# Optimization experiments

Hardware: AMD Instinct MI355X
Metric: run time of the kernel (lower is better)

The kernel has to match this reference:

```python
import jax, jax.numpy as jnp
import numpy as np

IN_FEATURES = 1024
ACT_BITS = 4


def _hadamard(size: int) -> np.ndarray:
    # Sylvester construction, normalized: H(n) = Sylvester(n) / sqrt(n)
    h = np.array([[1.0]], dtype=np.float64)
    while h.shape[0] < size:
        h = np.block([[h, h], [h, -h]])
    return (h / np.sqrt(size)).astype(np.float32)


def _quantize_activations(x, bits=ACT_BITS):
    pos = 2 ** (bits - 1) - 1  # 7
    neg = 2 ** (bits - 1)      # 8
    scale = jnp.clip(jnp.max(jnp.abs(jax.lax.stop_gradient(x)), axis=-1, keepdims=True), 1e-5) / pos
    q = jnp.clip(jnp.round(x / scale), -neg, pos) * scale
    return x + jax.lax.stop_gradient(q - x)  # STE


def _ternary_quantize_ste(w):
    scale = jnp.clip(jnp.mean(jnp.abs(jax.lax.stop_gradient(w)), axis=1, keepdims=True), 1e-5)
    n = w / scale
    tern = jnp.where(n > 0.5, 1.0, jnp.where(n < -0.5, -1.0, 0.0))
    q = tern * scale
    return w + jax.lax.stop_gradient(q - w)  # STE


def setup_inputs() -> dict:
    key = jax.random.key(0)
    k1, k2 = jax.random.split(key)
    x = jax.random.normal(k1, (8, 8192, IN_FEATURES), dtype=jnp.float32)
    # master weight ~ kaiming-uniform-ish scale
    bound = 1.0 / np.sqrt(IN_FEATURES)
    weight = jax.random.uniform(k2, (1024, IN_FEATURES), dtype=jnp.float32, minval=-bound, maxval=bound)
    return {"x": x, "weight": weight}


def reference(x, weight):
    H = jnp.asarray(_hadamard(IN_FEATURES))  # [in, in]
    xh = x @ H                                # Hadamard precondition on input
    xq = _quantize_activations(xh)            # per-token 4-bit symmetric quant (STE)
    wq = _ternary_quantize_ste(weight)        # per-row ternary quant (STE)
    return jnp.einsum('bsi,oi->bso', xq, wq)  # F.linear, no bias
```

## Files before the change

### kernel.cpp

```cpp
#include <hip/hip_runtime.h>
#include <stdint.h>

typedef int v4i __attribute__((ext_vector_type(4)));
typedef float float4_t __attribute__((ext_vector_type(4)));

#define K_DIM 1024
#define N_DIM 1024
#define BM 128
#define BN 128

__device__ __forceinline__ void gload16(const void* g, void* l) {
  __builtin_amdgcn_global_load_lds(
      (const __attribute__((address_space(1))) unsigned int*)g,
      (__attribute__((address_space(3))) unsigned int*)l, 16, 0, 0);
}

#define MFMA_I8 __builtin_amdgcn_mfma_i32_16x16x64_i8

__global__ __launch_bounds__(256) void fwht_quant_kernel(
    const float* __restrict__ x, int8_t* __restrict__ qx,
    float* __restrict__ ascale, int M) {
  const int lane = threadIdx.x & 63;
  const int wid = threadIdx.x >> 6;
  const long token = (long)blockIdx.x * 4 + wid;
  if (token >= M) return;
  const float4_t* xr4 = (const float4_t*)(x + token * K_DIM);

  float v[16];
#pragma unroll
  for (int i = 0; i < 4; ++i) {
    float4_t f = xr4[lane * 4 + i];
#pragma unroll
    for (int c = 0; c < 4; ++c) v[i * 4 + c] = f[c];
  }
#pragma unroll
  for (int s = 1; s <= 8; s <<= 1) {
#pragma unroll
    for (int r = 0; r < 16; ++r)
      if ((r & s) == 0) {
        float a0 = v[r], b0 = v[r | s];
        v[r] = a0 + b0;
        v[r | s] = a0 - b0;
      }
  }
#pragma unroll
  for (int m = 1; m <= 32; m <<= 1) {
    const float sg = (lane & m) ? -1.0f : 1.0f;
#pragma unroll
    for (int r = 0; r < 16; ++r) {
      float p = __shfl_xor(v[r], m, 64);
      v[r] = fmaf(sg, v[r], p);
    }
  }
  float mx = 0.f;
#pragma unroll
  for (int r = 0; r < 16; ++r) mx = fmaxf(mx, fabsf(v[r]));
#pragma unroll
  for (int m = 32; m >= 1; m >>= 1) mx = fmaxf(mx, __shfl_xor(mx, m, 64));
  const float scale = fmaxf(mx * 0.03125f, 1e-5f) * (1.0f / 7.0f);
  if (lane == 0) ascale[token] = scale;
  const float inv = 0.03125f / scale;

  v4i pk;
#pragma unroll
  for (int i = 0; i < 4; ++i) {
    int packed = 0;
#pragma unroll
    for (int c = 0; c < 4; ++c) {
      float q = rintf(v[i * 4 + c] * inv);
      q = fminf(7.f, fmaxf(-8.f, q));
      packed |= ((int)q & 0xff) << (8 * c);
    }
    pk[i] = packed;
  }
  *(v4i*)(qx + token * K_DIM + lane * 16) = pk;
}

__global__ __launch_bounds__(256) void wquant_kernel(
    const float* __restrict__ w, int8_t* __restrict__ qw,
    float* __restrict__ wscale) {
  const int lane = threadIdx.x & 63;
  const int wid = threadIdx.x >> 6;
  const int row = blockIdx.x * 4 + wid;
  const float* wr = w + (long)row * K_DIM;

  float v[16];
  float s = 0.f;
  const float4_t* wr4 = (const float4_t*)wr;
#pragma unroll
  for (int rr = 0; rr < 4; ++rr) {
    float4_t f = wr4[rr * 64 + lane];
#pragma unroll
    for (int c = 0; c < 4; ++c) {
      v[rr * 4 + c] = f[c];
      s += fabsf(f[c]);
    }
  }
#pragma unroll
  for (int m = 32; m >= 1; m >>= 1) s += __shfl_xor(s, m, 64);
  const float scale = fmaxf(s * (1.0f / 1024.0f), 1e-5f);
  if (lane == 0) wscale[row] = scale;

  int8_t* qr = qw + (long)row * K_DIM;
#pragma unroll
  for (int rr = 0; rr < 4; ++rr) {
    int packed = 0;
#pragma unroll
    for (int c = 0; c < 4; ++c) {
      float n = v[rr * 4 + c] / scale;
      int t = (n > 0.5f) ? 1 : ((n < -0.5f) ? -1 : 0);
      packed |= (t & 0xff) << (8 * c);
    }
    *(int*)(qr + rr * 256 + lane * 4) = packed;
  }
}

__global__ __launch_bounds__(256) void gemm_i8_kernel(
    const int8_t* __restrict__ A, const int8_t* __restrict__ B,
    const float* __restrict__ asc, const float* __restrict__ wsc,
    float* __restrict__ C, int M) {
  __shared__ __align__(16) int8_t smem[34816];
  int8_t* Al = smem;
  int8_t* Bl = smem + 16384;
  float* tr = (float*)smem;

  const int t = threadIdx.x;
  const int lane = t & 63;
  const int wm = (t >> 6) >> 1;
  const int wn = (t >> 6) & 1;
  const int rl = lane & 15;
  const int kb = lane >> 4;

  const int swz = ((int)blockIdx.x & 7) * 512 + ((int)blockIdx.x >> 3);
  const long bm = swz >> 3;
  const int bn = swz & 7;

  const int chunkoff = (((t & 7) ^ ((t >> 3) & 7)) << 4);
  const int8_t* gA = A + (bm * BM + (t >> 3)) * (long)K_DIM + chunkoff;
  const int8_t* gB = B + ((long)bn * BN + (t >> 3)) * K_DIM + chunkoff;

  const int sw0 = ((kb ^ (rl & 7)) << 4);
  const int sw1 = (((4 + kb) ^ (rl & 7)) << 4);
  const int arow = (wm * 64 + rl) * 128;
  const int brow = (wn * 64 + rl) * 128;

  v4i acc[4][4] = {};

  for (int ks = 0; ks < K_DIM; ks += 128) {
    gload16(gA + ks, Al + t * 16);
    gload16(gA + ks + 32 * K_DIM, Al + 4096 + t * 16);
    gload16(gA + ks + 64 * K_DIM, Al + 8192 + t * 16);
    gload16(gA + ks + 96 * K_DIM, Al + 12288 + t * 16);
    gload16(gB + ks, Bl + t * 16);
    gload16(gB + ks + 32 * K_DIM, Bl + 4096 + t * 16);
    gload16(gB + ks + 64 * K_DIM, Bl + 8192 + t * 16);
    gload16(gB + ks + 96 * K_DIM, Bl + 12288 + t * 16);
    __syncthreads();

#pragma unroll
    for (int ks2 = 0; ks2 < 2; ++ks2) {
      const int sw = ks2 ? sw1 : sw0;
      v4i a[4], b[4];
#pragma unroll
      for (int i = 0; i < 4; ++i)
        a[i] = *(const v4i*)(Al + arow + i * 2048 + sw);
#pragma unroll
      for (int j = 0; j < 4; ++j)
        b[j] = *(const v4i*)(Bl + brow + j * 2048 + sw);
#pragma unroll
      for (int i = 0; i < 4; ++i)
#pragma unroll
        for (int j = 0; j < 4; ++j)
          acc[i][j] = MFMA_I8(a[i], b[j], acc[i][j], 0, 0, 0);
    }
    __syncthreads();
  }

  const long rowg0 = bm * BM + wm * 64;
  const int colg0 = bn * BN + wn * 64;
#pragma unroll
  for (int c = 0; c < 2; ++c) {
    if (wm == c) {
#pragma unroll
      for (int i = 0; i < 4; ++i) {
        float as[4];
#pragma unroll
        for (int r = 0; r < 4; ++r) as[r] = asc[rowg0 + i * 16 + kb * 4 + r];
#pragma unroll
        for (int j = 0; j < 4; ++j) {
          const float ws = wsc[colg0 + j * 16 + rl];
#pragma unroll
          for (int r = 0; r < 4; ++r)
            tr[(i * 16 + kb * 4 + r) * 132 + wn * 64 + j * 16 + rl] =
                (float)acc[i][j][r] * as[r] * ws;
        }
      }
    }
    __syncthreads();
#pragma unroll
    for (int it = 0; it < 8; ++it) {
      const int idx = t + it * 256;
      const int rl2 = idx >> 5;
      const int c4 = (idx & 31) * 4;
      const float4_t val = *(const float4_t*)(tr + rl2 * 132 + c4);
      __builtin_nontemporal_store(
          val, (float4_t*)(C + (bm * BM + c * 64 + rl2) * (long)N_DIM + bn * BN + c4));
    }
    __syncthreads();
  }
}

extern "C" void kernel_launch(void* const* d_in, const int* in_sizes, int n_in,
                              void* d_out, int out_size, void* d_ws, size_t ws_size,
                              hipStream_t stream) {
  const float* x = (const float*)d_in[0];
  const float* w = (const float*)d_in[1];
  float* out = (float*)d_out;
  const int M = in_sizes[0] / K_DIM;

  int8_t* qx = (int8_t*)d_ws;
  int8_t* qw = qx + (size_t)M * K_DIM;
  float* ascale = (float*)(qw + (size_t)N_DIM * K_DIM);
  float* wscale = ascale + M;

  fwht_quant_kernel<<<(M + 3) / 4, 256, 0, stream>>>(x, qx, ascale, M);
  wquant_kernel<<<N_DIM / 4, 256, 0, stream>>>(w, qw, wscale);
  gemm_i8_kernel<<<(M / BM) * (N_DIM / BN), 256, 0, stream>>>(qx, qw, ascale, wscale, out, M);
}
```

Before: 172.8 us.

## Fuse Hadamard transform and activation quantization into the int8 GEMM kernel

Removes the standalone FWHT+quantize kernel and the int8 activation round trip through global memory. Each 512-thread block now transforms and quantizes a 64-token slab straight into LDS, keeping the whole K dimension resident. It then streams all 1024 weight columns through double-buffered LDS tiles, writing 64x128 output tiles as it goes. This cuts global traffic and one launch, but the smaller M tile means less MFMA reuse per B load, and each block reads all of B. The large LDS footprint limits occupancy to one block per CU.

```diff
diff --git a/kernel.cpp b/kernel.cpp
--- a/kernel.cpp
+++ b/kernel.cpp
@@ -6,8 +6,7 @@
 
 #define K_DIM 1024
 #define N_DIM 1024
-#define BM 128
-#define BN 128
+#define TOK 64
 
 __device__ __forceinline__ void gload16(const void* g, void* l) {
   __builtin_amdgcn_global_load_lds(
@@ -16,65 +15,6 @@
 }
 
 #define MFMA_I8 __builtin_amdgcn_mfma_i32_16x16x64_i8
-
-__global__ __launch_bounds__(256) void fwht_quant_kernel(
-    const float* __restrict__ x, int8_t* __restrict__ qx,
-    float* __restrict__ ascale, int M) {
-  const int lane = threadIdx.x & 63;
-  const int wid = threadIdx.x >> 6;
-  const long token = (long)blockIdx.x * 4 + wid;
-  if (token >= M) return;
-  const float4_t* xr4 = (const float4_t*)(x + token * K_DIM);
-
-  float v[16];
-#pragma unroll
-  for (int i = 0; i < 4; ++i) {
-    float4_t f = xr4[lane * 4 + i];
-#pragma unroll
-    for (int c = 0; c < 4; ++c) v[i * 4 + c] = f[c];
-  }
-#pragma unroll
-  for (int s = 1; s <= 8; s <<= 1) {
-#pragma unroll
-    for (int r = 0; r < 16; ++r)
-      if ((r & s) == 0) {
-        float a0 = v[r], b0 = v[r | s];
-        v[r] = a0 + b0;
-        v[r | s] = a0 - b0;
-      }
-  }
-#pragma unroll
-  for (int m = 1; m <= 32; m <<= 1) {
-    const float sg = (lane & m) ? -1.0f : 1.0f;
-#pragma unroll
-    for (int r = 0; r < 16; ++r) {
-      float p = __shfl_xor(v[r], m, 64);
-      v[r] = fmaf(sg, v[r], p);
-    }
-  }
-  float mx = 0.f;
-#pragma unroll
-  for (int r = 0; r < 16; ++r) mx = fmaxf(mx, fabsf(v[r]));
-#pragma unroll
-  for (int m = 32; m >= 1; m >>= 1) mx = fmaxf(mx, __shfl_xor(mx, m, 64));
-  const float scale = fmaxf(mx * 0.03125f, 1e-5f) * (1.0f / 7.0f);
-  if (lane == 0) ascale[token] = scale;
-  const float inv = 0.03125f / scale;
-
-  v4i pk;
-#pragma unroll
-  for (int i = 0; i < 4; ++i) {
-    int packed = 0;
-#pragma unroll
-    for (int c = 0; c < 4; ++c) {
-      float q = rintf(v[i * 4 + c] * inv);
-      q = fminf(7.f, fmaxf(-8.f, q));
-      packed |= ((int)q & 0xff) << (8 * c);
-    }
-    pk[i] = packed;
-  }
-  *(v4i*)(qx + token * K_DIM + lane * 16) = pk;
-}
 
 __global__ __launch_bounds__(256) void wquant_kernel(
     const float* __restrict__ w, int8_t* __restrict__ qw,
@@ -108,106 +48,177 @@
 #pragma unroll
     for (int c = 0; c < 4; ++c) {
       float n = v[rr * 4 + c] / scale;
-      int t = (n > 0.5f) ? 1 : ((n < -0.5f) ? -1 : 0);
-      packed |= (t & 0xff) << (8 * c);
+      int tv = (n > 0.5f) ? 1 : ((n < -0.5f) ? -1 : 0);
+      packed |= (tv & 0xff) << (8 * c);
     }
     *(int*)(qr + rr * 256 + lane * 4) = packed;
   }
 }
 
-__global__ __launch_bounds__(256) void gemm_i8_kernel(
-    const int8_t* __restrict__ A, const int8_t* __restrict__ B,
-    const float* __restrict__ asc, const float* __restrict__ wsc,
-    float* __restrict__ C, int M) {
-  __shared__ __align__(16) int8_t smem[34816];
-  int8_t* Al = smem;
-  int8_t* Bl = smem + 16384;
-  float* tr = (float*)smem;
+__global__ __launch_bounds__(512) void fused_fwht_gemm_kernel(
+    const float* __restrict__ x, const int8_t* __restrict__ Bq,
+    const float* __restrict__ wsc, float* __restrict__ C) {
+  __shared__ __align__(16) int8_t smem[132352];
+  int8_t* At = smem;
+  int8_t* Bb0 = smem + 65536;
+  int8_t* Bb1 = smem + 81920;
+  float* tr = (float*)(smem + 98304);
+  float* ascl = (float*)(smem + 132096);
 
   const int t = threadIdx.x;
   const int lane = t & 63;
-  const int wm = (t >> 6) >> 1;
-  const int wn = (t >> 6) & 1;
+  const int wid = t >> 6;
+  const int wm = wid >> 2;
+  const int wn = wid & 3;
   const int rl = lane & 15;
   const int kb = lane >> 4;
-
-  const int swz = ((int)blockIdx.x & 7) * 512 + ((int)blockIdx.x >> 3);
-  const long bm = swz >> 3;
-  const int bn = swz & 7;
+  const long bm = blockIdx.x;
+
+  {
+    const float4_t* xb = (const float4_t*)(x + bm * TOK * (long)K_DIM);
+    int token = wid * 8;
+    float4_t f0 = xb[(long)token * 256 + lane * 4 + 0];
+    float4_t f1 = xb[(long)token * 256 + lane * 4 + 1];
+    float4_t f2 = xb[(long)token * 256 + lane * 4 + 2];
+    float4_t f3 = xb[(long)token * 256 + lane * 4 + 3];
+    for (int tk = 0; tk < 8; ++tk) {
+      float4_t g0, g1, g2, g3;
+      if (tk < 7) {
+        g0 = xb[(long)(token + 1) * 256 + lane * 4 + 0];
+        g1 = xb[(long)(token + 1) * 256 + lane * 4 + 1];
+        g2 = xb[(long)(token + 1) * 256 + lane * 4 + 2];
+        g3 = xb[(long)(token + 1) * 256 + lane * 4 + 3];
+      }
+      float v[16];
+#pragma unroll
+      for (int c = 0; c < 4; ++c) {
+        v[c] = f0[c]; v[4 + c] = f1[c]; v[8 + c] = f2[c]; v[12 + c] = f3[c];
+      }
+#pragma unroll
+      for (int s = 1; s <= 8; s <<= 1) {
+#pragma unroll
+        for (int r = 0; r < 16; ++r)
+          if ((r & s) == 0) {
+            float a0 = v[r], b0 = v[r | s];
+            v[r] = a0 + b0;
+            v[r | s] = a0 - b0;
+          }
+      }
+#pragma unroll
+      for (int m = 1; m <= 32; m <<= 1) {
+        const float sg = (lane & m) ? -1.0f : 1.0f;
+#pragma unroll
+        for (int r = 0; r < 16; ++r) {
+          float p = __shfl_xor(v[r], m, 64);
+          v[r] = fmaf(sg, v[r], p);
+        }
+      }
+      float mx = 0.f;
+#pragma unroll
+      for (int r = 0; r < 16; ++r) mx = fmaxf(mx, fabsf(v[r]));
+#pragma unroll
+      for (int m = 32; m >= 1; m >>= 1) mx = fmaxf(mx, __shfl_xor(mx, m, 64));
+      const float scale = fmaxf(mx * 0.03125f, 1e-5f) * (1.0f / 7.0f);
+      if (lane == 0) ascl[token] = scale;
+      const float inv = 0.03125f / scale;
+
+      v4i pk;
+#pragma unroll
+      for (int i = 0; i < 4; ++i) {
+        int packed = 0;
+#pragma unroll
+        for (int c = 0; c < 4; ++c) {
+          float q = rintf(v[i * 4 + c] * inv);
+          q = fminf(7.f, fmaxf(-8.f, q));
+          packed |= ((int)q & 0xff) << (8 * c);
+        }
+        pk[i] = packed;
+      }
+      *(v4i*)(At + token * 1024 + ((lane >> 3) << 7) +
+              (((lane & 7) ^ (token & 7)) << 4)) = pk;
+      f0 = g0; f1 = g1; f2 = g2; f3 = g3;
+      ++token;
+    }
+  }
 
   const int chunkoff = (((t & 7) ^ ((t >> 3) & 7)) << 4);
-  const int8_t* gA = A + (bm * BM + (t >> 3)) * (long)K_DIM + chunkoff;
-  const int8_t* gB = B + ((long)bn * BN + (t >> 3)) * K_DIM + chunkoff;
-
   const int sw0 = ((kb ^ (rl & 7)) << 4);
   const int sw1 = (((4 + kb) ^ (rl & 7)) << 4);
-  const int arow = (wm * 64 + rl) * 128;
-  const int brow = (wn * 64 + rl) * 128;
-
-  v4i acc[4][4] = {};
-
-  for (int ks = 0; ks < K_DIM; ks += 128) {
-    gload16(gA + ks, Al + t * 16);
-    gload16(gA + ks + 32 * K_DIM, Al + 4096 + t * 16);
-    gload16(gA + ks + 64 * K_DIM, Al + 8192 + t * 16);
-    gload16(gA + ks + 96 * K_DIM, Al + 12288 + t * 16);
-    gload16(gB + ks, Bl + t * 16);
-    gload16(gB + ks + 32 * K_DIM, Bl + 4096 + t * 16);
-    gload16(gB + ks + 64 * K_DIM, Bl + 8192 + t * 16);
-    gload16(gB + ks + 96 * K_DIM, Bl + 12288 + t * 16);
+  const int arow0 = wm * 32 + rl;
+  const int bcol0 = wn * 32 + rl;
+
+  v4i acc[2][2] = {};
+
+#define STAGE(s_)                                                             \
+  {                                                                           \
+    const int bn_ = (s_) >> 3, kt_ = (s_) & 7;                                \
+    int8_t* dst = ((s_) & 1) ? Bb1 : Bb0;                                     \
+    const int8_t* gB = Bq + ((long)(bn_ * 128 + (t >> 3))) * K_DIM +          \
+                       kt_ * 128 + chunkoff;                                  \
+    gload16(gB, dst + t * 16);                                                \
+    gload16(gB + 64 * K_DIM, dst + 8192 + t * 16);                            \
+  }
+
+  STAGE(0);
+  __syncthreads();
+
+  for (int s = 0; s < 64; ++s) {
+    const int kt = s & 7;
+    if (s < 63) STAGE(s + 1);
+    const int8_t* Bl = (s & 1) ? Bb1 : Bb0;
+    v4i a[2][2], b[2][2];
+#pragma unroll
+    for (int i = 0; i < 2; ++i) {
+      a[i][0] = *(const v4i*)(At + (arow0 + i * 16) * 1024 + kt * 128 + sw0);
+      a[i][1] = *(const v4i*)(At + (arow0 + i * 16) * 1024 + kt * 128 + sw1);
+    }
+#pragma unroll
+    for (int j = 0; j < 2; ++j) {
+      b[j][0] = *(const v4i*)(Bl + (bcol0 + j * 16) * 128 + sw0);
+      b[j][1] = *(const v4i*)(Bl + (bcol0 + j * 16) * 128 + sw1);
+    }
+#pragma unroll
+    for (int i = 0; i < 2; ++i)
+#pragma unroll
+      for (int j = 0; j < 2; ++j) {
+        acc[i][j] = MFMA_I8(a[i][0], b[j][0], acc[i][j], 0, 0, 0);
+        acc[i][j] = MFMA_I8(a[i][1], b[j][1], acc[i][j], 0, 0, 0);
+      }
     __syncthreads();
 
-#pragma unroll
-    for (int ks2 = 0; ks2 < 2; ++ks2) {
-      const int sw = ks2 ? sw1 : sw0;
-      v4i a[4], b[4];
-#pragma unroll
-      for (int i = 0; i < 4; ++i)
-        a[i] = *(const v4i*)(Al + arow + i * 2048 + sw);
-#pragma unroll
-      for (int j = 0; j < 4; ++j)
-        b[j] = *(const v4i*)(Bl + brow + j * 2048 + sw);
-#pragma unroll
-      for (int i = 0; i < 4; ++i)
-#pragma unroll
-        for (int j = 0; j < 4; ++j)
-          acc[i][j] = MFMA_I8(a[i], b[j], acc[i][j], 0, 0, 0);
-    }
-    __syncthreads();
-  }
-
-  const long rowg0 = bm * BM + wm * 64;
-  const int colg0 = bn * BN + wn * 64;
-#pragma unroll
-  for (int c = 0; c < 2; ++c) {
-    if (wm == c) {
-#pragma unroll
-      for (int i = 0; i < 4; ++i) {
+    if (kt == 7) {
+      const int bn = s >> 3;
+#pragma unroll
+      for (int i = 0; i < 2; ++i) {
         float as[4];
 #pragma unroll
-        for (int r = 0; r < 4; ++r) as[r] = asc[rowg0 + i * 16 + kb * 4 + r];
-#pragma unroll
-        for (int j = 0; j < 4; ++j) {
-          const float ws = wsc[colg0 + j * 16 + rl];
+        for (int r = 0; r < 4; ++r) as[r] = ascl[wm * 32 + i * 16 + kb * 4 + r];
+#pragma unroll
+        for (int j = 0; j < 2; ++j) {
+          const float ws = wsc[bn * 128 + wn * 32 + j * 16 + rl];
 #pragma unroll
           for (int r = 0; r < 4; ++r)
-            tr[(i * 16 + kb * 4 + r) * 132 + wn * 64 + j * 16 + rl] =
+            tr[(wm * 32 + i * 16 + kb * 4 + r) * 132 + wn * 32 + j * 16 + rl] =
                 (float)acc[i][j][r] * as[r] * ws;
         }
       }
-    }
-    __syncthreads();
-#pragma unroll
-    for (int it = 0; it < 8; ++it) {
-      const int idx = t + it * 256;
-      const int rl2 = idx >> 5;
-      const int c4 = (idx & 31) * 4;
-      const float4_t val = *(const float4_t*)(tr + rl2 * 132 + c4);
-      __builtin_nontemporal_store(
-          val, (float4_t*)(C + (bm * BM + c * 64 + rl2) * (long)N_DIM + bn * BN + c4));
-    }
-    __syncthreads();
-  }
+      __syncthreads();
+#pragma unroll
+      for (int it = 0; it < 4; ++it) {
+        const int idx = t + it * 512;
+        const int row = idx >> 5;
+        const int c4 = (idx & 31) * 4;
+        __builtin_nontemporal_store(
+            *(const float4_t*)(tr + row * 132 + c4),
+            (float4_t*)(C + (bm * TOK + row) * (long)N_DIM + bn * 128 + c4));
+      }
+#pragma unroll
+      for (int i = 0; i < 2; ++i)
+#pragma unroll
+        for (int j = 0; j < 2; ++j) acc[i][j] = (v4i){0, 0, 0, 0};
+    }
+  }
+#undef STAGE
 }
 
 extern "C" void kernel_launch(void* const* d_in, const int* in_sizes, int n_in,
@@ -218,12 +229,9 @@
   float* out = (float*)d_out;
   const int M = in_sizes[0] / K_DIM;
 
-  int8_t* qx = (int8_t*)d_ws;
-  int8_t* qw = qx + (size_t)M * K_DIM;
-  float* ascale = (float*)(qw + (size_t)N_DIM * K_DIM);
-  float* wscale = ascale + M;
-
-  fwht_quant_kernel<<<(M + 3) / 4, 256, 0, stream>>>(x, qx, ascale, M);
+  int8_t* qw = (int8_t*)d_ws;
+  float* wscale = (float*)(qw + (size_t)N_DIM * K_DIM);
+
   wquant_kernel<<<N_DIM / 4, 256, 0, stream>>>(w, qw, wscale);
-  gemm_i8_kernel<<<(M / BM) * (N_DIM / BN), 256, 0, stream>>>(qx, qw, ascale, wscale, out, M);
-}
+  fused_fwht_gemm_kernel<<<M / TOK, 512, 0, stream>>>(x, qw, wscale, out);
+}
```

Measured after the change: 266.7 us. +54.3%, slower.
